# Optimization experiments

Measured on AMD Instinct MI355X. Metric: run time of the kernel, lower is better.

## Reference

```python
import jax, jax.numpy as jnp
import numpy as np

IN_C, HID, OUT = 3, 128, 256
K1, K2 = 16, 8
N = 8192


def _knn_idx(x, k):
    # x: [N, C] -> indices of k nearest neighbors (excluding self), [N, k]
    n = x.shape[0]
    sq = jnp.sum(x * x, axis=1)
    d = sq[:, None] + sq[None, :] - 2.0 * (x @ x.T)  # [N, N] squared dists
    i = jnp.arange(n)
    d = d.at[i, i].set(jnp.inf)  # loop=False: exclude self
    _, idx = jax.lax.top_k(-d, k)
    return idx


def _edge_conv(x, W1, b1, W2, b2, k):
    # DynamicEdgeConv: knn graph on x, edge feat [x_i, x_j - x_i], MLP, max aggr
    n, c = x.shape
    idx = _knn_idx(x, k)              # [N, k]
    xj = x[idx]                       # [N, k, C]
    xi = x[:, None, :]                # [N, 1, C]
    e = jnp.concatenate([jnp.broadcast_to(xi, (n, k, c)), xj - xi], axis=-1)  # [N, k, 2C]
    h = jax.nn.relu(e @ W1 + b1) @ W2 + b2  # [N, k, H]
    return jnp.max(h, axis=1)               # max aggregation -> [N, H]


def setup_inputs() -> dict:
    key = jax.random.key(0)
    ks = jax.random.split(key, 9)
    def lin(k, fan_in, fan_out):
        bound = 1.0 / np.sqrt(fan_in)
        kw, kb = jax.random.split(k)
        W = jax.random.uniform(kw, (fan_in, fan_out), jnp.float32, -bound, bound)
        b = jax.random.uniform(kb, (fan_out,), jnp.float32, -bound, bound)
        return W, b
    x = jax.random.normal(ks[0], (N, IN_C), jnp.float32)
    W1a, b1a = lin(ks[1], 2 * IN_C, HID)
    W1b, b1b = lin(ks[2], HID, HID)
    W2a, b2a = lin(ks[3], 2 * HID, OUT)
    W2b, b2b = lin(ks[4], OUT, OUT)
    return {"x": x, "W1a": W1a, "b1a": b1a, "W1b": W1b, "b1b": b1b,
            "W2a": W2a, "b2a": b2a, "W2b": W2b, "b2b": b2b}


def reference(x, W1a, b1a, W1b, b1b, W2a, b2a, W2b, b2b):
    h = _edge_conv(x, W1a, b1a, W1b, b1b, K1)   # [N, HID]
    out = _edge_conv(h, W2a, b2a, W2b, b2b, K2)  # [N, OUT]
    return out
```

## Files before the change

kernel.cpp:

```cpp
#include <hip/hip_runtime.h>
#include <math.h>

constexpr int NPTS  = 8192;
constexpr int HIDC  = 128;
constexpr int OUTC2 = 256;
constexpr int PQC   = 512;
constexpr int KK1   = 16;
constexpr int KK2   = 8;

typedef __attribute__((ext_vector_type(8))) short short8;
typedef __attribute__((ext_vector_type(4))) float f32x4;

__device__ __forceinline__ f32x4 mfma16(short8 a, short8 b, f32x4 c) {
  return __builtin_amdgcn_mfma_f32_16x16x32_bf16(a, b, c, 0, 0, 0);
}

__device__ __forceinline__ void async_ld16(void* lds, const void* g) {
  __builtin_amdgcn_global_load_lds(
      (const __attribute__((address_space(1))) unsigned int*)g,
      (__attribute__((address_space(3))) unsigned int*)lds, 16, 0, 0);
}

template <int K>
__device__ __forceinline__ void ins_u(unsigned (&kk)[K], unsigned v) {
  if (v < kk[K - 1]) {
    kk[K - 1] = v;
    #pragma unroll
    for (int p = K - 1; p > 0; --p) {
      unsigned a = kk[p - 1], b = kk[p];
      kk[p - 1] = a < b ? a : b;
      kk[p]     = a < b ? b : a;
    }
  }
}

template <int K>
__device__ __forceinline__ void ins_lex(float (&kf)[K], int (&ki)[K], float v, int j) {
  bool ins = (v < kf[K - 1]) || (v == kf[K - 1] && j < ki[K - 1]);
  if (ins) {
    kf[K - 1] = v; ki[K - 1] = j;
    #pragma unroll
    for (int p = K - 1; p > 0; --p) {
      float fa = kf[p - 1], fb = kf[p];
      int   ia = ki[p - 1], ib = ki[p];
      bool sw = (fb < fa) || (fb == fa && ib < ia);
      kf[p - 1] = sw ? fb : fa; ki[p - 1] = sw ? ib : ia;
      kf[p]     = sw ? fa : fb; ki[p]     = sw ? ia : ib;
    }
  }
}

__device__ __forceinline__ unsigned short bf16_rn(float x) {
  unsigned int u = __float_as_uint(x);
  unsigned int r = u + 0x7fffu + ((u >> 16) & 1u);
  return (unsigned short)(r >> 16);
}

__global__ void pack_x_kernel(const float* __restrict__ x, float4* __restrict__ x4) {
  int i = blockIdx.x * blockDim.x + threadIdx.x;
  if (i < NPTS) {
    float a = x[3 * i], b = x[3 * i + 1], c = x[3 * i + 2];
    x4[i] = make_float4(a, b, c, a * a + b * b + c * c);
  }
}

__global__ void prep_w1_kernel(const float* __restrict__ W1, float* __restrict__ Wc) {
  int idx = blockIdx.x * 256 + threadIdx.x;
  int k = idx >> 9, c = idx & 511;
  float wh = W1[(size_t)(HIDC + k) * OUTC2 + (c & 255)];
  Wc[idx] = (c < OUTC2) ? (W1[(size_t)k * OUTC2 + c] - wh) : wh;
}

__global__ void prep_w2_kernel(const float* __restrict__ W2,
                               unsigned short* __restrict__ W2Fhi,
                               unsigned short* __restrict__ W2Flo) {
  const int c = blockIdx.x;
  const int k = threadIdx.x;
  float w = W2[(size_t)k * OUTC2 + c];
  unsigned short hi = bf16_rn(w);
  float fh = __uint_as_float(((unsigned int)hi) << 16);
  unsigned short lo = bf16_rn(w - fh);
  const int nt = c >> 4, ct = c & 15;
  const int s  = k >> 5, kg = (k >> 3) & 3, e = k & 7;
  const int lane = kg * 16 + ct;
  const size_t idx = ((size_t)(s * 16 + nt) * 64 + lane) * 8 + e;
  W2Fhi[idx] = hi;
  W2Flo[idx] = lo;
}

__global__ __launch_bounds__(256) void knn3_kernel(const float4* __restrict__ X4,
                                                   int* __restrict__ idx_out) {
  const int tid  = threadIdx.x;
  const int lane = tid & 63;
  const int wv   = __builtin_amdgcn_readfirstlane(tid >> 6);
  const int q    = blockIdx.x * 4 + wv;

  const float4 qv = X4[q];

  unsigned kk[KK2];
  #pragma unroll
  for (int k = 0; k < KK2; ++k) kk[k] = 0xFFFFFFFFu;

  for (int c = 0; c < NPTS / 64; ++c) {
    const int j = c * 64 + lane;
    float4 pj = X4[j];
    float d = fmaxf(qv.w + pj.w - 2.f * (qv.x * pj.x + qv.y * pj.y + qv.z * pj.z), 0.f);
    unsigned key = (__float_as_uint(d) & 0xFFFFE000u) | (unsigned)j;
    if (j == q) key = 0xFFFFFFFFu;
    ins_u<KK2>(kk, key);
  }

  float kf[KK2]; int kj[KK2];
  #pragma unroll
  for (int k = 0; k < KK2; ++k) { kf[k] = INFINITY; kj[k] = 0x7fffffff; }
  #pragma unroll
  for (int k = 0; k < KK2; ++k) {
    int j = (int)(kk[k] & 0x1FFFu);
    float4 pj = X4[j];
    float d = qv.w + pj.w - 2.f * (qv.x * pj.x + qv.y * pj.y + qv.z * pj.z);
    if (kk[k] == 0xFFFFFFFFu) { d = INFINITY; j = 0x7fffffff; }
    ins_lex<KK2>(kf, kj, d, j);
  }

  #pragma unroll
  for (int k = 0; k < KK1; ++k) {
    float mf = kf[0]; int mj = kj[0];
    #pragma unroll
    for (int m = 1; m <= 32; m <<= 1) {
      float of = __shfl_xor(mf, m, 64);
      int   oj = __shfl_xor(mj, m, 64);
      bool g = (of < mf) || (of == mf && oj < mj);
      mf = g ? of : mf; mj = g ? oj : mj;
    }
    const bool won = (kf[0] == mf) && (kj[0] == mj);
    if (won) {
      idx_out[(size_t)q * KK1 + k] = mj;
      #pragma unroll
      for (int p = 0; p < KK2 - 1; ++p) { kf[p] = kf[p + 1]; kj[p] = kj[p + 1]; }
      kf[KK2 - 1] = INFINITY; kj[KK2 - 1] = 0x7fffffff;
    }
  }
}

__global__ __launch_bounds__(256) void edgeconv1_kernel(
    const float* __restrict__ X, const int* __restrict__ knn,
    const float* __restrict__ W1, const float* __restrict__ b1,
    const float* __restrict__ W2, const float* __restrict__ b2,
    float* __restrict__ H, unsigned short* __restrict__ Hhi,
    unsigned short* __restrict__ Hlo, float* __restrict__ SQ2) {
  __shared__ float h1[8][KK1][HIDC];
  __shared__ float xjs[8][KK1][3];
  __shared__ float xis[8][3];
  const int tid  = threadIdx.x;
  const int lane = tid & 63;
  const int wv   = __builtin_amdgcn_readfirstlane(tid >> 6);
  const int half = lane >> 5;
  const int hl   = lane & 31;
  const int lp   = wv * 2 + half;
  const int p    = blockIdx.x * 8 + lp;
  const int ch0  = hl * 4;

  if (hl < KK1) {
    int j = knn[p * KK1 + hl];
    xjs[lp][hl][0] = X[3 * j]; xjs[lp][hl][1] = X[3 * j + 1]; xjs[lp][hl][2] = X[3 * j + 2];
  } else if (hl < KK1 + 3) {
    xis[lp][hl - KK1] = X[3 * p + hl - KK1];
  }
  __syncthreads();

  f32x4 w1r[6];
  #pragma unroll
  for (int c = 0; c < 6; ++c) w1r[c] = *(const f32x4*)&W1[c * HIDC + ch0];
  f32x4 b1v = *(const f32x4*)&b1[ch0];
  const float xi0 = xis[lp][0], xi1 = xis[lp][1], xi2 = xis[lp][2];
  f32x4 base;
  #pragma unroll
  for (int c = 0; c < 4; ++c)
    base[c] = b1v[c] + xi0 * w1r[0][c] + xi1 * w1r[1][c] + xi2 * w1r[2][c];
  #pragma unroll
  for (int e = 0; e < KK1; ++e) {
    float dx = xjs[lp][e][0] - xi0, dy = xjs[lp][e][1] - xi1, dz = xjs[lp][e][2] - xi2;
    f32x4 v;
    #pragma unroll
    for (int c = 0; c < 4; ++c)
      v[c] = fmaxf(base[c] + dx * w1r[3][c] + dy * w1r[4][c] + dz * w1r[5][c], 0.f);
    *(f32x4*)&h1[lp][e][ch0] = v;
  }
  __syncthreads();

  float acc[KK1][4];
  #pragma unroll
  for (int e = 0; e < KK1; ++e)
    #pragma unroll
    for (int c = 0; c < 4; ++c) acc[e][c] = 0.f;
  for (int c4 = 0; c4 < HIDC / 4; ++c4) {
    f32x4 w2r[4];
    #pragma unroll
    for (int cc = 0; cc < 4; ++cc)
      w2r[cc] = *(const f32x4*)&W2[(c4 * 4 + cc) * HIDC + ch0];
    #pragma unroll
    for (int e = 0; e < KK1; ++e) {
      f32x4 hv = *(const f32x4*)&h1[lp][e][c4 * 4];
      #pragma unroll
      for (int cc = 0; cc < 4; ++cc)
        #pragma unroll
        for (int c = 0; c < 4; ++c) acc[e][c] += hv[cc] * w2r[cc][c];
    }
  }
  f32x4 b2v = *(const f32x4*)&b2[ch0];
  f32x4 outv;
  #pragma unroll
  for (int c = 0; c < 4; ++c) {
    float m = -INFINITY;
    #pragma unroll
    for (int e = 0; e < KK1; ++e) m = fmaxf(m, acc[e][c]);
    outv[c] = m + b2v[c];
  }
  *(f32x4*)&H[(size_t)p * HIDC + ch0] = outv;

  unsigned short hb[4], lb[4];
  #pragma unroll
  for (int c = 0; c < 4; ++c) {
    hb[c] = bf16_rn(outv[c]);
    float fh = __uint_as_float(((unsigned int)hb[c]) << 16);
    lb[c] = bf16_rn(outv[c] - fh);
  }
  *(ushort4*)&Hhi[(size_t)p * HIDC + ch0] = make_ushort4(hb[0], hb[1], hb[2], hb[3]);
  *(ushort4*)&Hlo[(size_t)p * HIDC + ch0] = make_ushort4(lb[0], lb[1], lb[2], lb[3]);

  float s = outv[0]*outv[0] + outv[1]*outv[1] + outv[2]*outv[2] + outv[3]*outv[3];
  #pragma unroll
  for (int m = 1; m <= 16; m <<= 1) s += __shfl_xor(s, m, 64);
  if (hl == 0) SQ2[p] = s;
}

__global__ __launch_bounds__(256) void gemm_pq_kernel(
    const float* __restrict__ H, const float* __restrict__ Wc,
    const float* __restrict__ b1, float* __restrict__ PQ) {
  __shared__ float Hs[32][HIDC];
  const int tid = threadIdx.x;
  const int rb  = blockIdx.x >> 3;
  const int cb  = blockIdx.x & 7;
  const int col = cb * 64 + (tid & 63);
  const int rg  = tid >> 6;

  #pragma unroll
  for (int u = 0; u < 4; ++u) {
    int idx = u * 256 + tid;
    int r = idx >> 5, k4 = idx & 31;
    *(f32x4*)&Hs[r][k4 * 4] = *(const f32x4*)&H[(size_t)(rb * 32 + r) * HIDC + k4 * 4];
  }
  __syncthreads();

  float acc[8] = {};
  for (int k = 0; k < HIDC; ++k) {
    float w = Wc[(size_t)k * PQC + col];
    #pragma unroll
    for (int i = 0; i < 8; ++i) acc[i] += Hs[rg * 8 + i][k] * w;
  }
  const float bb = (col < OUTC2) ? b1[col] : 0.f;
  #pragma unroll
  for (int i = 0; i < 8; ++i)
    PQ[(size_t)(rb * 32 + rg * 8 + i) * PQC + col] = acc[i] + bb;
}

constexpr int JSPLIT = 16;
constexpr int JPB2   = NPTS / JSPLIT;
constexpr int NCH    = JPB2 / 16;
constexpr int CPQ    = JSPLIT * KK2;

__global__ __launch_bounds__(256) void knn128_filter_kernel(
    const unsigned short* __restrict__ Hhi, const unsigned short* __restrict__ Hlo,
    const float* __restrict__ SQ, unsigned* __restrict__ pk2) {
  __shared__ __align__(16) unsigned short As[2][2][16 * HIDC];
  const int tid  = threadIdx.x;
  const int lane = tid & 63;
  const int wv   = __builtin_amdgcn_readfirstlane(tid >> 6);
  const int qb   = blockIdx.x >> 4;
  const int js   = blockIdx.x & 15;
  const int col  = lane & 15;
  const int kg   = lane >> 4;
  const int qg   = qb * 64 + wv * 16 + col;

  short8 qhi[4], qlo[4];
  #pragma unroll
  for (int s = 0; s < 4; ++s) {
    const size_t o = (size_t)qg * HIDC + s * 32 + kg * 8;
    qhi[s] = *reinterpret_cast<const short8*>(Hhi + o);
    qlo[s] = *reinterpret_cast<const short8*>(Hlo + o);
  }
  const float sqq = SQ[qg];

  unsigned kk[KK2];
  #pragma unroll
  for (int k = 0; k < KK2; ++k) kk[k] = 0xFFFFFFFFu;

  const int jbase = js * JPB2;

  const int srow = 4 * wv + (lane >> 4);
  const int sslt = (lane & 15) ^ (srow & 7);
  auto stage = [&](int buf, int ch) {
    const size_t gofs = (size_t)(jbase + ch * 16 + srow) * HIDC + sslt * 8;
    async_ld16((char*)&As[buf][0][0] + wv * 1024, Hhi + gofs);
    async_ld16((char*)&As[buf][1][0] + wv * 1024, Hlo + gofs);
  };

  stage(0, 0);
  asm volatile("s_waitcnt vmcnt(0)" ::: "memory");
  __syncthreads();

  for (int ch = 0; ch < NCH; ++ch) {
    const int cur = ch & 1;
    if (ch + 1 < NCH) stage(cur ^ 1, ch + 1);

    const int jb = jbase + ch * 16;
    short8 ahi[4], alo[4];
    const int rowb = col * 256;
    #pragma unroll
    for (int s = 0; s < 4; ++s) {
      const int sl = ((s * 4 + kg) ^ (col & 7)) * 16;
      ahi[s] = *(const short8*)((const char*)&As[cur][0][0] + rowb + sl);
      alo[s] = *(const short8*)((const char*)&As[cur][1][0] + rowb + sl);
    }
    f32x4 sqjv = *reinterpret_cast<const f32x4*>(SQ + jb + kg * 4);

    f32x4 acc = {0.f, 0.f, 0.f, 0.f};
    #pragma unroll
    for (int s = 0; s < 4; ++s) {
      acc = mfma16(ahi[s], qhi[s], acc);
      acc = mfma16(ahi[s], qlo[s], acc);
      acc = mfma16(alo[s], qhi[s], acc);
    }
    #pragma unroll
    for (int r = 0; r < 4; ++r) {
      const int jg = jb + kg * 4 + r;
      float d = fmaxf(sqq + sqjv[r] - 2.f * acc[r], 0.f);
      unsigned key = (__float_as_uint(d) & 0xFFFFE000u) | (unsigned)jg;
      if (jg == qg) key = 0xFFFFFFFFu;
      ins_u<KK2>(kk, key);
    }
    asm volatile("s_waitcnt vmcnt(0)" ::: "memory");
    __syncthreads();
  }

  #pragma unroll
  for (int dlt = 16; dlt <= 32; dlt <<= 1) {
    unsigned ok[KK2];
    #pragma unroll
    for (int k = 0; k < KK2; ++k) ok[k] = __shfl_xor((int)kk[k], dlt, 64);
    #pragma unroll
    for (int k = 0; k < KK2; ++k) ins_u<KK2>(kk, ok[k]);
  }
  if (lane < 16) {
    const size_t base = (size_t)qg * CPQ + js * KK2;
    #pragma unroll
    for (int k = 0; k < KK2; ++k) pk2[base + k] = kk[k];
  }
}

__global__ __launch_bounds__(256) void knn_rescore_kernel(
    const float* __restrict__ H, const float* __restrict__ SQ,
    const unsigned* __restrict__ pk2, int* __restrict__ idx_out) {
  __shared__ float qrow[16][HIDC + 4];
  const int tid  = threadIdx.x;
  const int lane = tid & 63;
  const int wv   = tid >> 6;
  const int g    = lane >> 4;
  const int sl   = lane & 15;
  const int q0   = blockIdx.x * 16;
  const int qloc = wv * 4 + g;
  const int q    = q0 + qloc;

  for (int u = tid; u < 16 * 32; u += 256) {
    int r = u >> 5, c4 = u & 31;
    *(f32x4*)&qrow[r][c4 * 4] = *(const f32x4*)&H[(size_t)(q0 + r) * HIDC + c4 * 4];
  }
  __syncthreads();

  unsigned kreg[KK2];
  {
    const unsigned* src = pk2 + (size_t)q * CPQ + sl * KK2;
    uint4 a = *(const uint4*)(src);
    uint4 b = *(const uint4*)(src + 4);
    kreg[0] = a.x; kreg[1] = a.y; kreg[2] = a.z; kreg[3] = a.w;
    kreg[4] = b.x; kreg[5] = b.y; kreg[6] = b.z; kreg[7] = b.w;
  }

  unsigned ckey = 0xFFFFFFFFu;
  #pragma unroll
  for (int t = 0; t < 16; ++t) {
    unsigned m = kreg[0];
    #pragma unroll
    for (int mm = 1; mm <= 8; mm <<= 1) {
      unsigned o = (unsigned)__shfl_xor((int)m, mm, 64);
      m = o < m ? o : m;
    }
    if (t == sl) ckey = m;
    const bool won = (kreg[0] == m);
    if (won) {
      #pragma unroll
      for (int p = 0; p < KK2 - 1; ++p) kreg[p] = kreg[p + 1];
      kreg[KK2 - 1] = 0xFFFFFFFFu;
    }
  }
  const int ci = (int)(ckey & 0x1FFFu);

  const float* crow = H + (size_t)ci * HIDC;
  float dot = 0.f;
  #pragma unroll 8
  for (int c4 = 0; c4 < HIDC / 4; ++c4) {
    f32x4 qv = *(const f32x4*)&qrow[qloc][c4 * 4];
    f32x4 cv = *(const f32x4*)(crow + c4 * 4);
    dot += qv[0] * cv[0] + qv[1] * cv[1] + qv[2] * cv[2] + qv[3] * cv[3];
  }
  float d = SQ[q] + SQ[ci] - 2.f * dot;

  float kf[KK2]; int ki[KK2];
  kf[0] = d; ki[0] = ci;
  #pragma unroll
  for (int k = 1; k < KK2; ++k) { kf[k] = INFINITY; ki[k] = 0x7fffffff; }
  #pragma unroll
  for (int dlt = 1; dlt <= 8; dlt <<= 1) {
    float of[KK2]; int oi[KK2];
    #pragma unroll
    for (int k = 0; k < KK2; ++k) { of[k] = __shfl_xor(kf[k], dlt, 64); oi[k] = __shfl_xor(ki[k], dlt, 64); }
    #pragma unroll
    for (int k = 0; k < KK2; ++k) ins_lex<KK2>(kf, ki, of[k], oi[k]);
  }
  if (sl == 0) {
    #pragma unroll
    for (int k = 0; k < KK2; ++k) idx_out[(size_t)q * KK2 + k] = ki[k];
  }
}

__global__ __launch_bounds__(512) void edgeconv2_kernel(
    const float* __restrict__ PQ, const int* __restrict__ knn,
    const unsigned short* __restrict__ W2Fhi, const unsigned short* __restrict__ W2Flo,
    const float* __restrict__ b2, float* __restrict__ Out) {
  __shared__ __align__(16) unsigned short Ghi[64 * OUTC2];
  __shared__ __align__(16) unsigned short Glo[64 * OUTC2];
  __shared__ __align__(16) unsigned short Bs[2][2][8192];
  const int tid  = threadIdx.x;
  const int lane = tid & 63;
  const int wv   = __builtin_amdgcn_readfirstlane(tid >> 6);
  const int p_base = blockIdx.x * 8;

  {
    const int p   = p_base + wv;
    const int ch0 = lane * 4;
    f32x4 pv = *(const f32x4*)&PQ[(size_t)p * PQC + ch0];
    #pragma unroll
    for (int e = 0; e < KK2; ++e) {
      const int j = knn[p * KK2 + e];
      f32x4 qv = *(const f32x4*)&PQ[(size_t)j * PQC + OUTC2 + ch0];
      unsigned short hb[4], lb[4];
      #pragma unroll
      for (int c = 0; c < 4; ++c) {
        float g = fmaxf(pv[c] + qv[c], 0.f);
        hb[c] = bf16_rn(g);
        float fh = __uint_as_float(((unsigned int)hb[c]) << 16);
        lb[c] = bf16_rn(g - fh);
      }
      const int r   = wv * 8 + e;
      const int off = r * 512 + (((ch0 >> 3) ^ (r & 7)) << 4) + ((ch0 & 7) << 1);
      *(ushort4*)((char*)Ghi + off) = make_ushort4(hb[0], hb[1], hb[2], hb[3]);
      *(ushort4*)((char*)Glo + off) = make_ushort4(lb[0], lb[1], lb[2], lb[3]);
    }
  }

  auto stageB = [&](int buf, int s) {
    #pragma unroll
    for (int i = 0; i < 2; ++i) {
      const size_t go = (size_t)s * 8192 + (size_t)(wv * 2 + i) * 512 + (size_t)lane * 8;
      async_ld16((char*)&Bs[buf][0][0] + (wv * 2 + i) * 1024, W2Fhi + go);
      async_ld16((char*)&Bs[buf][1][0] + (wv * 2 + i) * 1024, W2Flo + go);
    }
  };

  stageB(0, 0);
  asm volatile("s_waitcnt vmcnt(0)" ::: "memory");
  __syncthreads();

  const int col = lane & 15;
  const int kg  = lane >> 4;
  const int mt  = wv & 3;
  const int nh  = wv >> 2;
  const int ar  = mt * 16 + col;
  const int abase = ar * 512;

  f32x4 acc[8];
  #pragma unroll
  for (int n = 0; n < 8; ++n) acc[n] = (f32x4){0.f, 0.f, 0.f, 0.f};

  for (int s = 0; s < 8; ++s) {
    const int cur = s & 1;
    if (s + 1 < 8) stageB(cur ^ 1, s + 1);

    const int asl = (((s * 4 + kg) ^ (ar & 7)) << 4);
    short8 ghi = *(const short8*)((const char*)Ghi + abase + asl);
    short8 glo = *(const short8*)((const char*)Glo + abase + asl);
    #pragma unroll
    for (int n = 0; n < 8; ++n) {
      const int nt = nh * 8 + n;
      const int bo = (nt * 64 + lane) * 16;
      short8 bhi = *(const short8*)((const char*)&Bs[cur][0][0] + bo);
      short8 blo = *(const short8*)((const char*)&Bs[cur][1][0] + bo);
      acc[n] = mfma16(ghi, bhi, acc[n]);
      acc[n] = mfma16(ghi, blo, acc[n]);
      acc[n] = mfma16(glo, bhi, acc[n]);
    }
    asm volatile("s_waitcnt vmcnt(0)" ::: "memory");
    __syncthreads();
  }

  const int pt = p_base + mt * 2 + (kg >> 1);
  #pragma unroll
  for (int n = 0; n < 8; ++n) {
    float m = fmaxf(fmaxf(acc[n][0], acc[n][1]), fmaxf(acc[n][2], acc[n][3]));
    m = fmaxf(m, __shfl_xor(m, 16, 64));
    if ((kg & 1) == 0) {
      const int ncol = nh * 128 + n * 16 + col;
      Out[(size_t)pt * OUTC2 + ncol] = m + b2[ncol];
    }
  }
}

extern "C" void kernel_launch(void* const* d_in, const int* in_sizes, int n_in,
                              void* d_out, int out_size, void* d_ws, size_t ws_size,
                              hipStream_t stream) {
  const float* x   = (const float*)d_in[0];
  const float* W1a = (const float*)d_in[1];
  const float* b1a = (const float*)d_in[2];
  const float* W1b = (const float*)d_in[3];
  const float* b1b = (const float*)d_in[4];
  const float* W2a = (const float*)d_in[5];
  const float* b2a = (const float*)d_in[6];
  const float* W2b = (const float*)d_in[7];
  const float* b2b = (const float*)d_in[8];
  float* out = (float*)d_out;

  float* h    = (float*)d_ws;
  float* sq2  = h + (size_t)NPTS * HIDC;
  int*   idx1 = (int*)(sq2 + NPTS);
  int*   idx2 = idx1 + (size_t)NPTS * KK1;
  unsigned short* Hhi = (unsigned short*)(idx2 + (size_t)NPTS * KK2);
  unsigned short* Hlo = Hhi + (size_t)NPTS * HIDC;
  unsigned* pk2 = (unsigned*)(Hlo + (size_t)NPTS * HIDC);
  float* Wc   = (float*)(pk2 + (size_t)NPTS * CPQ);
  float* PQ   = Wc + (size_t)HIDC * PQC;
  unsigned short* W2Fhi = (unsigned short*)(PQ + (size_t)NPTS * PQC);
  unsigned short* W2Flo = W2Fhi + (size_t)OUTC2 * OUTC2;
  float4* x4 = (float4*)h;

  pack_x_kernel<<<(NPTS + 255) / 256, 256, 0, stream>>>(x, x4);
  prep_w1_kernel<<<(HIDC * PQC) / 256, 256, 0, stream>>>(W2a, Wc);
  prep_w2_kernel<<<OUTC2, OUTC2, 0, stream>>>(W2b, W2Fhi, W2Flo);
  knn3_kernel<<<NPTS / 4, 256, 0, stream>>>(x4, idx1);
  edgeconv1_kernel<<<NPTS / 8, 256, 0, stream>>>(x, idx1, W1a, b1a, W1b, b1b,
                                                 h, Hhi, Hlo, sq2);
  gemm_pq_kernel<<<(NPTS / 32) * 8, 256, 0, stream>>>(h, Wc, b2a, PQ);
  knn128_filter_kernel<<<(NPTS / 64) * JSPLIT, 256, 0, stream>>>(Hhi, Hlo, sq2, pk2);
  knn_rescore_kernel<<<NPTS / 16, 256, 0, stream>>>(h, sq2, pk2, idx2);
  edgeconv2_kernel<<<NPTS / 8, 512, 0, stream>>>(PQ, idx2, W2Fhi, W2Flo, b2b, out);
}
```

Measured before the change: 303.6 us.

## Move edgeconv1 second layer and PQ GEMM onto split-bf16 MFMA

Replaces the scalar FP32 inner GEMM in edgeconv1 (16 edges by 128 channels per point) and the FP32 gemm_pq kernel with bf16 MFMA, using a hi/lo bf16 split and three MFMAs per tile to approximate FP32 accuracy. New prep kernels pre-swizzle the W1b and Wc weights into MFMA fragment layout. Tiles are staged into LDS with async global_load_lds and double buffering, and the A tiles use an XOR-swizzled LDS layout. This aims to cut ALU time on the two dense stages, at the cost of some precision (the hi*lo products are dropped) and larger LDS use per block.

Measured after the change: 269.1 us. -11.4%, faster.

```diff
diff --git a/kernel.cpp b/kernel.cpp
--- a/kernel.cpp
+++ b/kernel.cpp
@@ -64,11 +64,37 @@
   }
 }
 
-__global__ void prep_w1_kernel(const float* __restrict__ W1, float* __restrict__ Wc) {
+__global__ void prep_w1f_kernel(const float* __restrict__ W1,
+                                unsigned short* __restrict__ WcFhi,
+                                unsigned short* __restrict__ WcFlo) {
   int idx = blockIdx.x * 256 + threadIdx.x;
   int k = idx >> 9, c = idx & 511;
   float wh = W1[(size_t)(HIDC + k) * OUTC2 + (c & 255)];
-  Wc[idx] = (c < OUTC2) ? (W1[(size_t)k * OUTC2 + c] - wh) : wh;
+  float w = (c < OUTC2) ? (W1[(size_t)k * OUTC2 + c] - wh) : wh;
+  unsigned short hi = bf16_rn(w);
+  float fh = __uint_as_float(((unsigned int)hi) << 16);
+  unsigned short lo = bf16_rn(w - fh);
+  const int nt = c >> 4, ct = c & 15;
+  const int s = k >> 5, kg = (k >> 3) & 3, e = k & 7;
+  const size_t fidx = ((size_t)(s * 32 + nt) * 64 + (kg * 16 + ct)) * 8 + e;
+  WcFhi[fidx] = hi;
+  WcFlo[fidx] = lo;
+}
+
+__global__ void prep_w1b_kernel(const float* __restrict__ W,
+                                unsigned short* __restrict__ Fhi,
+                                unsigned short* __restrict__ Flo) {
+  const int c = blockIdx.x;
+  const int k = threadIdx.x;
+  float w = W[(size_t)k * HIDC + c];
+  unsigned short hi = bf16_rn(w);
+  float fh = __uint_as_float(((unsigned int)hi) << 16);
+  unsigned short lo = bf16_rn(w - fh);
+  const int nt = c >> 4, ct = c & 15;
+  const int s = k >> 5, kg = (k >> 3) & 3, e = k & 7;
+  const size_t idx = ((size_t)(s * 8 + nt) * 64 + (kg * 16 + ct)) * 8 + e;
+  Fhi[idx] = hi;
+  Flo[idx] = lo;
 }
 
 __global__ void prep_w2_kernel(const float* __restrict__ W2,
@@ -142,126 +168,196 @@
   }
 }
 
-__global__ __launch_bounds__(256) void edgeconv1_kernel(
+__global__ __launch_bounds__(512) void edgeconv1_kernel(
     const float* __restrict__ X, const int* __restrict__ knn,
     const float* __restrict__ W1, const float* __restrict__ b1,
-    const float* __restrict__ W2, const float* __restrict__ b2,
+    const unsigned short* __restrict__ W1bFhi, const unsigned short* __restrict__ W1bFlo,
+    const float* __restrict__ b2,
     float* __restrict__ H, unsigned short* __restrict__ Hhi,
     unsigned short* __restrict__ Hlo, float* __restrict__ SQ2) {
-  __shared__ float h1[8][KK1][HIDC];
+  __shared__ __align__(16) unsigned short Ghi[128 * HIDC];
+  __shared__ __align__(16) unsigned short Glo[128 * HIDC];
+  __shared__ __align__(16) unsigned short Bs[2][2][4096];
   __shared__ float xjs[8][KK1][3];
   __shared__ float xis[8][3];
   const int tid  = threadIdx.x;
   const int lane = tid & 63;
   const int wv   = __builtin_amdgcn_readfirstlane(tid >> 6);
-  const int half = lane >> 5;
-  const int hl   = lane & 31;
-  const int lp   = wv * 2 + half;
-  const int p    = blockIdx.x * 8 + lp;
-  const int ch0  = hl * 4;
-
-  if (hl < KK1) {
-    int j = knn[p * KK1 + hl];
-    xjs[lp][hl][0] = X[3 * j]; xjs[lp][hl][1] = X[3 * j + 1]; xjs[lp][hl][2] = X[3 * j + 2];
-  } else if (hl < KK1 + 3) {
-    xis[lp][hl - KK1] = X[3 * p + hl - KK1];
+  const int p    = blockIdx.x * 8 + wv;
+
+  if (lane < KK1) {
+    int j = knn[p * KK1 + lane];
+    xjs[wv][lane][0] = X[3 * j]; xjs[wv][lane][1] = X[3 * j + 1]; xjs[wv][lane][2] = X[3 * j + 2];
+  } else if (lane < KK1 + 3) {
+    xis[wv][lane - KK1] = X[3 * p + lane - KK1];
   }
   __syncthreads();
 
-  f32x4 w1r[6];
-  #pragma unroll
-  for (int c = 0; c < 6; ++c) w1r[c] = *(const f32x4*)&W1[c * HIDC + ch0];
-  f32x4 b1v = *(const f32x4*)&b1[ch0];
-  const float xi0 = xis[lp][0], xi1 = xis[lp][1], xi2 = xis[lp][2];
-  f32x4 base;
-  #pragma unroll
-  for (int c = 0; c < 4; ++c)
-    base[c] = b1v[c] + xi0 * w1r[0][c] + xi1 * w1r[1][c] + xi2 * w1r[2][c];
-  #pragma unroll
-  for (int e = 0; e < KK1; ++e) {
-    float dx = xjs[lp][e][0] - xi0, dy = xjs[lp][e][1] - xi1, dz = xjs[lp][e][2] - xi2;
-    f32x4 v;
-    #pragma unroll
-    for (int c = 0; c < 4; ++c)
-      v[c] = fmaxf(base[c] + dx * w1r[3][c] + dy * w1r[4][c] + dz * w1r[5][c], 0.f);
-    *(f32x4*)&h1[lp][e][ch0] = v;
-  }
+  {
+    const int ch0 = lane * 2;
+    float2 w1r[6];
+    #pragma unroll
+    for (int c = 0; c < 6; ++c)
+      w1r[c] = make_float2(W1[c * HIDC + ch0], W1[c * HIDC + ch0 + 1]);
+    const float2 b1v = make_float2(b1[ch0], b1[ch0 + 1]);
+    const float xi0 = xis[wv][0], xi1 = xis[wv][1], xi2 = xis[wv][2];
+    const float base0 = b1v.x + xi0 * w1r[0].x + xi1 * w1r[1].x + xi2 * w1r[2].x;
+    const float base1 = b1v.y + xi0 * w1r[0].y + xi1 * w1r[1].y + xi2 * w1r[2].y;
+    #pragma unroll
+    for (int e = 0; e < KK1; ++e) {
+      float dx = xjs[wv][e][0] - xi0, dy = xjs[wv][e][1] - xi1, dz = xjs[wv][e][2] - xi2;
+      float v0 = fmaxf(base0 + dx * w1r[3].x + dy * w1r[4].x + dz * w1r[5].x, 0.f);
+      float v1 = fmaxf(base1 + dx * w1r[3].y + dy * w1r[4].y + dz * w1r[5].y, 0.f);
+      unsigned short h0 = bf16_rn(v0), h1s = bf16_rn(v1);
+      unsigned short l0 = bf16_rn(v0 - __uint_as_float(((unsigned)h0) << 16));
+      unsigned short l1 = bf16_rn(v1 - __uint_as_float(((unsigned)h1s) << 16));
+      const int r   = wv * 16 + e;
+      const int off = r * 256 + (((ch0 >> 3) ^ (r & 7)) << 4) + ((ch0 & 7) << 1);
+      *(ushort2*)((char*)Ghi + off) = make_ushort2(h0, h1s);
+      *(ushort2*)((char*)Glo + off) = make_ushort2(l0, l1);
+    }
+  }
+
+  auto stageB = [&](int buf, int s) {
+    const size_t go = (size_t)s * 4096 + (size_t)wv * 512 + (size_t)lane * 8;
+    async_ld16((char*)&Bs[buf][0][0] + wv * 1024, W1bFhi + go);
+    async_ld16((char*)&Bs[buf][1][0] + wv * 1024, W1bFlo + go);
+  };
+
+  stageB(0, 0);
+  asm volatile("s_waitcnt vmcnt(0)" ::: "memory");
   __syncthreads();
 
-  float acc[KK1][4];
-  #pragma unroll
-  for (int e = 0; e < KK1; ++e)
-    #pragma unroll
-    for (int c = 0; c < 4; ++c) acc[e][c] = 0.f;
-  for (int c4 = 0; c4 < HIDC / 4; ++c4) {
-    f32x4 w2r[4];
-    #pragma unroll
-    for (int cc = 0; cc < 4; ++cc)
-      w2r[cc] = *(const f32x4*)&W2[(c4 * 4 + cc) * HIDC + ch0];
-    #pragma unroll
-    for (int e = 0; e < KK1; ++e) {
-      f32x4 hv = *(const f32x4*)&h1[lp][e][c4 * 4];
-      #pragma unroll
-      for (int cc = 0; cc < 4; ++cc)
-        #pragma unroll
-        for (int c = 0; c < 4; ++c) acc[e][c] += hv[cc] * w2r[cc][c];
-    }
-  }
-  f32x4 b2v = *(const f32x4*)&b2[ch0];
-  f32x4 outv;
-  #pragma unroll
-  for (int c = 0; c < 4; ++c) {
-    float m = -INFINITY;
-    #pragma unroll
-    for (int e = 0; e < KK1; ++e) m = fmaxf(m, acc[e][c]);
-    outv[c] = m + b2v[c];
-  }
-  *(f32x4*)&H[(size_t)p * HIDC + ch0] = outv;
-
-  unsigned short hb[4], lb[4];
-  #pragma unroll
-  for (int c = 0; c < 4; ++c) {
-    hb[c] = bf16_rn(outv[c]);
-    float fh = __uint_as_float(((unsigned int)hb[c]) << 16);
-    lb[c] = bf16_rn(outv[c] - fh);
-  }
-  *(ushort4*)&Hhi[(size_t)p * HIDC + ch0] = make_ushort4(hb[0], hb[1], hb[2], hb[3]);
-  *(ushort4*)&Hlo[(size_t)p * HIDC + ch0] = make_ushort4(lb[0], lb[1], lb[2], lb[3]);
-
-  float s = outv[0]*outv[0] + outv[1]*outv[1] + outv[2]*outv[2] + outv[3]*outv[3];
-  #pragma unroll
-  for (int m = 1; m <= 16; m <<= 1) s += __shfl_xor(s, m, 64);
-  if (hl == 0) SQ2[p] = s;
-}
-
-__global__ __launch_bounds__(256) void gemm_pq_kernel(
-    const float* __restrict__ H, const float* __restrict__ Wc,
+  const int col = lane & 15;
+  const int kg  = lane >> 4;
+  const int ar  = wv * 16 + col;
+  const int abase = ar * 256;
+
+  f32x4 acc[8];
+  #pragma unroll
+  for (int n = 0; n < 8; ++n) acc[n] = (f32x4){0.f, 0.f, 0.f, 0.f};
+
+  for (int s = 0; s < 4; ++s) {
+    const int cur = s & 1;
+    if (s + 1 < 4) stageB(cur ^ 1, s + 1);
+    const int asl = (((s * 4 + kg) ^ (ar & 7)) << 4);
+    short8 ghi = *(const short8*)((const char*)Ghi + abase + asl);
+    short8 glo = *(const short8*)((const char*)Glo + abase + asl);
+    #pragma unroll
+    for (int n = 0; n < 8; ++n) {
+      const int bo = (n * 64 + lane) * 16;
+      short8 bhi = *(const short8*)((const char*)&Bs[cur][0][0] + bo);
+      short8 blo = *(const short8*)((const char*)&Bs[cur][1][0] + bo);
+      acc[n] = mfma16(ghi, bhi, acc[n]);
+      acc[n] = mfma16(ghi, blo, acc[n]);
+      acc[n] = mfma16(glo, bhi, acc[n]);
+    }
+    asm volatile("s_waitcnt vmcnt(0)" ::: "memory");
+    __syncthreads();
+  }
+
+  float sq = 0.f;
+  float hv[8];
+  #pragma unroll
+  for (int n = 0; n < 8; ++n) {
+    float m = fmaxf(fmaxf(acc[n][0], acc[n][1]), fmaxf(acc[n][2], acc[n][3]));
+    m = fmaxf(m, __shfl_xor(m, 16, 64));
+    m = fmaxf(m, __shfl_xor(m, 32, 64));
+    m += b2[n * 16 + col];
+    hv[n] = m;
+    sq += m * m;
+  }
+  if (kg == 0) {
+    #pragma unroll
+    for (int n = 0; n < 8; ++n) {
+      const int ch = n * 16 + col;
+      H[(size_t)p * HIDC + ch] = hv[n];
+      unsigned short hb = bf16_rn(hv[n]);
+      float fh = __uint_as_float(((unsigned)hb) << 16);
+      Hhi[(size_t)p * HIDC + ch] = hb;
+      Hlo[(size_t)p * HIDC + ch] = bf16_rn(hv[n] - fh);
+    }
+  }
+  #pragma unroll
+  for (int m2 = 1; m2 <= 8; m2 <<= 1) sq += __shfl_xor(sq, m2, 64);
+  if (lane == 0) SQ2[p] = sq;
+}
+
+__global__ __launch_bounds__(512) void gemm_pq_kernel(
+    const unsigned short* __restrict__ Hhi, const unsigned short* __restrict__ Hlo,
+    const unsigned short* __restrict__ WcFhi, const unsigned short* __restrict__ WcFlo,
     const float* __restrict__ b1, float* __restrict__ PQ) {
-  __shared__ float Hs[32][HIDC];
-  const int tid = threadIdx.x;
-  const int rb  = blockIdx.x >> 3;
-  const int cb  = blockIdx.x & 7;
-  const int col = cb * 64 + (tid & 63);
-  const int rg  = tid >> 6;
-
-  #pragma unroll
-  for (int u = 0; u < 4; ++u) {
-    int idx = u * 256 + tid;
-    int r = idx >> 5, k4 = idx & 31;
-    *(f32x4*)&Hs[r][k4 * 4] = *(const f32x4*)&H[(size_t)(rb * 32 + r) * HIDC + k4 * 4];
-  }
+  __shared__ __align__(16) unsigned short Ahi[64 * HIDC];
+  __shared__ __align__(16) unsigned short Alo[64 * HIDC];
+  __shared__ __align__(16) unsigned short Bsl[2][2][8192];
+  const int tid  = threadIdx.x;
+  const int lane = tid & 63;
+  const int wv   = __builtin_amdgcn_readfirstlane(tid >> 6);
+  const int mb   = blockIdx.x >> 1;
+  const int ns   = blockIdx.x & 1;
+  const int r0   = mb * 64;
+
+  #pragma unroll
+  for (int i = 0; i < 2; ++i) {
+    const int srow = wv * 8 + i * 4 + (lane >> 4);
+    const int sslt = (lane & 15) ^ (srow & 7);
+    const size_t go = (size_t)(r0 + srow) * HIDC + sslt * 8;
+    async_ld16((char*)Ahi + (wv * 8 + i * 4) * 256, Hhi + go);
+    async_ld16((char*)Alo + (wv * 8 + i * 4) * 256, Hlo + go);
+  }
+  auto stageB = [&](int buf, int s) {
+    #pragma unroll
+    for (int i = 0; i < 2; ++i) {
+      const size_t go = (size_t)(s * 32 + ns * 16) * 512 + (size_t)wv * 1024 + i * 512 + lane * 8;
+      async_ld16((char*)&Bsl[buf][0][0] + wv * 2048 + i * 1024, WcFhi + go);
+      async_ld16((char*)&Bsl[buf][1][0] + wv * 2048 + i * 1024, WcFlo + go);
+    }
+  };
+  stageB(0, 0);
+  asm volatile("s_waitcnt vmcnt(0)" ::: "memory");
   __syncthreads();
 
-  float acc[8] = {};
-  for (int k = 0; k < HIDC; ++k) {
-    float w = Wc[(size_t)k * PQC + col];
-    #pragma unroll
-    for (int i = 0; i < 8; ++i) acc[i] += Hs[rg * 8 + i][k] * w;
-  }
-  const float bb = (col < OUTC2) ? b1[col] : 0.f;
-  #pragma unroll
-  for (int i = 0; i < 8; ++i)
-    PQ[(size_t)(rb * 32 + rg * 8 + i) * PQC + col] = acc[i] + bb;
+  const int col = lane & 15;
+  const int kg  = lane >> 4;
+  const int mt  = wv & 3;
+  const int nh  = wv >> 2;
+  const int ar  = mt * 16 + col;
+  const int abase = ar * 256;
+
+  f32x4 acc[8];
+  #pragma unroll
+  for (int n = 0; n < 8; ++n) acc[n] = (f32x4){0.f, 0.f, 0.f, 0.f};
+
+  for (int s = 0; s < 4; ++s) {
+    const int cur = s & 1;
+    if (s + 1 < 4) stageB(cur ^ 1, s + 1);
+    const int asl = (((s * 4 + kg) ^ (ar & 7)) << 4);
+    short8 ahi8 = *(const short8*)((const char*)Ahi + abase + asl);
+    short8 alo8 = *(const short8*)((const char*)Alo + abase + asl);
+    #pragma unroll
+    for (int n = 0; n < 8; ++n) {
+      const int ntl = nh * 8 + n;
+      const int bo = (ntl * 64 + lane) * 16;
+      short8 bhi = *(const short8*)((const char*)&Bsl[cur][0][0] + bo);
+      short8 blo = *(const short8*)((const char*)&Bsl[cur][1][0] + bo);
+      acc[n] = mfma16(ahi8, bhi, acc[n]);
+      acc[n] = mfma16(ahi8, blo, acc[n]);
+      acc[n] = mfma16(alo8, bhi, acc[n]);
+    }
+    asm volatile("s_waitcnt vmcnt(0)" ::: "memory");
+    __syncthreads();
+  }
+
+  #pragma unroll
+  for (int n = 0; n < 8; ++n) {
+    const int cg = ns * 256 + (nh * 8 + n) * 16 + col;
+    const float bb = (ns == 0) ? b1[cg] : 0.f;
+    #pragma unroll
+    for (int r = 0; r < 4; ++r) {
+      const int row = r0 + mt * 16 + kg * 4 + r;
+      PQ[(size_t)row * PQC + cg] = acc[n][r] + bb;
+    }
+  }
 }
 
 constexpr int JSPLIT = 16;
@@ -546,19 +642,24 @@
   unsigned short* Hhi = (unsigned short*)(idx2 + (size_t)NPTS * KK2);
   unsigned short* Hlo = Hhi + (size_t)NPTS * HIDC;
   unsigned* pk2 = (unsigned*)(Hlo + (size_t)NPTS * HIDC);
-  float* Wc   = (float*)(pk2 + (size_t)NPTS * CPQ);
-  float* PQ   = Wc + (size_t)HIDC * PQC;
+  float* PQ   = (float*)(pk2 + (size_t)NPTS * CPQ);
   unsigned short* W2Fhi = (unsigned short*)(PQ + (size_t)NPTS * PQC);
   unsigned short* W2Flo = W2Fhi + (size_t)OUTC2 * OUTC2;
+  unsigned short* WcFhi = W2Flo + (size_t)OUTC2 * OUTC2;
+  unsigned short* WcFlo = WcFhi + (size_t)HIDC * PQC;
+  unsigned short* W1bFhi = WcFlo + (size_t)HIDC * PQC;
+  unsigned short* W1bFlo = W1bFhi + (size_t)HIDC * HIDC;
   float4* x4 = (float4*)h;
 
   pack_x_kernel<<<(NPTS + 255) / 256, 256, 0, stream>>>(x, x4);
-  prep_w1_kernel<<<(HIDC * PQC) / 256, 256, 0, stream>>>(W2a, Wc);
+  prep_w1f_kernel<<<(HIDC * PQC) / 256, 256, 0, stream>>>(W2a, WcFhi, WcFlo);
+  prep_w1b_kernel<<<HIDC, HIDC, 0, stream>>>(W1b, W1bFhi, W1bFlo);
   prep_w2_kernel<<<OUTC2, OUTC2, 0, stream>>>(W2b, W2Fhi, W2Flo);
   knn3_kernel<<<NPTS / 4, 256, 0, stream>>>(x4, idx1);
-  edgeconv1_kernel<<<NPTS / 8, 256, 0, stream>>>(x, idx1, W1a, b1a, W1b, b1b,
+  edgeconv1_kernel<<<NPTS / 8, 512, 0, stream>>>(x, idx1, W1a, b1a,
+                                                 W1bFhi, W1bFlo, b1b,
                                                  h, Hhi, Hlo, sq2);
-  gemm_pq_kernel<<<(NPTS / 32) * 8, 256, 0, stream>>>(h, Wc, b2a, PQ);
+  gemm_pq_kernel<<<(NPTS / 64) * 2, 512, 0, stream>>>(Hhi, Hlo, WcFhi, WcFlo, b2a, PQ);
   knn128_filter_kernel<<<(NPTS / 64) * JSPLIT, 256, 0, stream>>>(Hhi, Hlo, sq2, pk2);
   knn_rescore_kernel<<<NPTS / 16, 256, 0, stream>>>(h, sq2, pk2, idx2);
   edgeconv2_kernel<<<NPTS / 8, 512, 0, stream>>>(PQ, idx2, W2Fhi, W2Flo, b2b, out);
```
